# Kernel optimization log

Hardware: AMD Instinct MI355X
Metric: run time of the kernel (lower is better)

Reference implementation:

```python
import jax, jax.numpy as jnp
import numpy as np

B, T, D, HD = 4, 4096, 1024, 64

def setup_inputs() -> dict:
    key = jax.random.key(0)
    k1, k2, k3, k4 = jax.random.split(key, 4)
    scale = 1.0 / np.sqrt(D)
    return {
        "x": jax.random.normal(k1, (B, T, D), dtype=jnp.float32),
        "Wq": jax.random.normal(k2, (HD, D), dtype=jnp.float32) * scale,
        "Wk": jax.random.normal(k3, (HD, D), dtype=jnp.float32) * scale,
        "Wv": jax.random.normal(k4, (HD, D), dtype=jnp.float32) * scale,
    }

def reference(x, Wq, Wk, Wv):
    # x: [B,T,D]; W*: [head_dim, D] (torch Linear weight layout)
    Q = jnp.einsum('btd,hd->bth', x, Wq)  # [B,T,HD]
    K = jnp.einsum('btd,hd->bth', x, Wk)
    V = jnp.einsum('btd,hd->bth', x, Wv)
    hd = Q.shape[-1]
    scores = jnp.einsum('bqh,bkh->bqk', Q, K) * (hd ** -0.5)  # [B,T,T]
    t = scores.shape[1]
    causal = jnp.tril(jnp.ones((t, t), dtype=bool))
    scores = jnp.where(causal, scores, -jnp.inf)
    att = jax.nn.softmax(scores, axis=-1)
    return jnp.einsum('bqk,bkh->bqh', att, V)  # [B,T,HD]
```

## Files before the change

kernel.cpp:

```cpp
#include <hip/hip_runtime.h>
#include <stdint.h>

#define B_  4
#define T_  4096
#define D_  1024
#define HD_ 64
#define BT_ 16384

typedef short bf16x8 __attribute__((ext_vector_type(8)));
typedef float f32x4  __attribute__((ext_vector_type(4)));
typedef float f32x16 __attribute__((ext_vector_type(16)));
typedef unsigned short u16;
typedef u16 u16x4 __attribute__((ext_vector_type(4)));
typedef unsigned int u32;
typedef u32 u32x4 __attribute__((ext_vector_type(4)));

#define M0L2_  11.54156032f
#define QSCALE_ 0.18033688f

#define CPB_   264
#define NSLOT_ (4 * CPB_ * 2)

__device__ __forceinline__ u16 f2bf(float f) {
    union { float f; unsigned u; } v; v.f = f;
    unsigned r = (v.u + 0x7FFF + ((v.u >> 16) & 1)) >> 16;
    return (u16)r;
}
__device__ __forceinline__ float bf2f(u16 u) {
    union { unsigned u; float f; } v; v.u = ((unsigned)u) << 16;
    return v.f;
}
__device__ __forceinline__ u32 cvt_pk_bf16(float lo, float hi) {
    u32 r;
    asm("v_cvt_pk_bf16_f32 %0, %1, %2" : "=v"(r) : "v"(lo), "v"(hi));
    return r;
}

__global__ __launch_bounds__(256) void wconv_kernel(
    const float* __restrict__ wq, const float* __restrict__ wk,
    const float* __restrict__ wv, u16* __restrict__ wb)
{
    const int j   = blockIdx.x >> 5;
    const int off = (blockIdx.x & 31) * 2048 + threadIdx.x * 8;
    const float* src = (j == 0) ? wq : ((j == 1) ? wk : wv);
    f32x4 a0 = *(const f32x4*)(src + off);
    f32x4 a1 = *(const f32x4*)(src + off + 4);
    u32x4 b;
    b[0] = cvt_pk_bf16(a0[0], a0[1]);
    b[1] = cvt_pk_bf16(a0[2], a0[3]);
    b[2] = cvt_pk_bf16(a1[0], a1[1]);
    b[3] = cvt_pk_bf16(a1[2], a1[3]);
    *(u32x4*)(wb + j * 65536 + off) = b;
}

__global__ __launch_bounds__(256) void qkv_kernel(
    const float* __restrict__ x, const u16* __restrict__ wb,
    u16* __restrict__ qs, u16* __restrict__ kss, u16* __restrict__ vssT)
{
    __shared__ __align__(16) u16 xt[32][72];
    __shared__ __align__(16) u16 wt[192][72];

    const int tid  = threadIdx.x;
    const int lane = tid & 63;
    const int w    = tid >> 6;
    const int quad = lane >> 4;
    const int l16  = lane & 15;
    const int row0 = blockIdx.x * 32;
    const int sp   = w >> 1;
    const int gh   = (w & 1) * 6;

    const int xrow = tid >> 3;
    const int xcg  = tid & 7;

    f32x4 acc[6];
    #pragma unroll
    for (int g = 0; g < 6; ++g) acc[g] = (f32x4)0.0f;

    f32x4 xa, xb;
    bf16x8 wr[6];
    {
        const float* xp = x + (size_t)(row0 + xrow) * D_ + xcg * 8;
        xa = *(const f32x4*)xp; xb = *(const f32x4*)(xp + 4);
        #pragma unroll
        for (int i = 0; i < 6; ++i) {
            int chunk = tid + 256 * i;
            wr[i] = *(const bf16x8*)(wb + (size_t)(chunk >> 3) * D_ + (chunk & 7) * 8);
        }
    }

    for (int kc = 0; kc < 16; ++kc) {
        __syncthreads();
        {
            u32x4 px;
            px[0] = cvt_pk_bf16(xa[0], xa[1]);
            px[1] = cvt_pk_bf16(xa[2], xa[3]);
            px[2] = cvt_pk_bf16(xb[0], xb[1]);
            px[3] = cvt_pk_bf16(xb[2], xb[3]);
            *(u32x4*)&xt[xrow][xcg * 8] = px;
            #pragma unroll
            for (int i = 0; i < 6; ++i) {
                int chunk = tid + 256 * i;
                *(bf16x8*)&wt[chunk >> 3][(chunk & 7) * 8] = wr[i];
            }
        }
        __syncthreads();
        if (kc < 15) {
            const float* xp = x + (size_t)(row0 + xrow) * D_ + (kc + 1) * 64 + xcg * 8;
            xa = *(const f32x4*)xp; xb = *(const f32x4*)(xp + 4);
            #pragma unroll
            for (int i = 0; i < 6; ++i) {
                int chunk = tid + 256 * i;
                wr[i] = *(const bf16x8*)(wb + (size_t)(chunk >> 3) * D_ + (kc + 1) * 64 + (chunk & 7) * 8);
            }
        }
        #pragma unroll
        for (int ks = 0; ks < 2; ++ks) {
            bf16x8 a = *(const bf16x8*)&xt[sp * 16 + l16][ks * 32 + quad * 8];
            #pragma unroll
            for (int g = 0; g < 6; ++g) {
                bf16x8 b = *(const bf16x8*)&wt[(gh + g) * 16 + l16][ks * 32 + quad * 8];
                acc[g] = __builtin_amdgcn_mfma_f32_16x16x32_bf16(a, b, acc[g], 0, 0, 0);
            }
        }
    }
    #pragma unroll
    for (int g = 0; g < 6; ++g) {
        const int n = (gh + g) * 16 + l16;
        const int j = n >> 6, h = n & 63;
        const int rbase = row0 + sp * 16 + quad * 4;
        if (j == 0) {
            #pragma unroll
            for (int r = 0; r < 4; ++r) qs[(size_t)(rbase + r) * HD_ + h] = f2bf(acc[g][r] * QSCALE_);
        } else if (j == 1) {
            #pragma unroll
            for (int r = 0; r < 4; ++r) kss[(size_t)(rbase + r) * HD_ + h] = f2bf(acc[g][r]);
        } else {
            u16x4 v;
            #pragma unroll
            for (int r = 0; r < 4; ++r) v[r] = f2bf(acc[g][r]);
            *(u16x4*)(vssT + (size_t)h * BT_ + rbase) = v;
        }
    }
}

__global__ __launch_bounds__(256, 4) void attn_kernel(
    const u16* __restrict__ qs, const u16* __restrict__ kss,
    const u16* __restrict__ vssT,
    float* __restrict__ pl, u16* __restrict__ pO)
{
    __shared__ __align__(16) u16 kt2[8 * 65 * 8];
    __shared__ __align__(16) u16 vt2[8 * 65 * 8];

    const int m = blockIdx.x % CPB_;
    const int b = blockIdx.x / CPB_;

    int t0, bound, qtA, qtB;
    if (m < 240)      { int u = m >> 4; t0 = (m & 15) * 4; bound = 2 * u + 2; qtA = u;  qtB = 30 - u; }
    else if (m < 248) { t0 = (m - 240) * 4; bound = 1 << 30; qtA = 15; qtB = 15; }
    else              { t0 = (m - 248) * 4; bound = 1 << 30; qtA = 31; qtB = 31; }

    const int tid  = threadIdx.x;
    const int lane = tid & 63;
    const int w    = tid >> 6;
    const int l31  = lane & 31;
    const int hi   = lane >> 5;
    const size_t base = (size_t)b * T_;

    int qt    = (t0 < bound) ? qtA : qtB;
    int kti   = (t0 < bound) ? t0 : (t0 - bound);
    int qrow0 = qt * 128 + w * 32;

    bf16x8 qf[4];
    #pragma unroll
    for (int ds = 0; ds < 4; ++ds)
        qf[ds] = *(const bf16x8*)(qs + (base + qrow0 + l31) * HD_ + ds * 16 + hi * 8);

    f32x16 o0 = (f32x16)0.0f, o1 = (f32x16)0.0f;
    float l_acc = 0.0f;

    const int srow = tid >> 2, q4 = tid & 3;
    const u16* kp = kss  + (base + srow) * HD_ + q4 * 16;
    const u16* vp = vssT + (size_t)srow * BT_ + base + q4 * 16;
    u16* kdst = kt2 + ((((srow >> 5) * 4 + q4) * 65 + (srow & 31)) * 8);
    u16* vdst = vt2 + ((((srow >> 5) * 4 + q4) * 65 + (srow & 31)) * 8);

    bf16x8 kr0, kr1, vr0, vr1;
    {
        const u16* k0 = kp + (size_t)kti * 64 * HD_;
        kr0 = *(const bf16x8*)k0; kr1 = *(const bf16x8*)(k0 + 8);
        const u16* v0 = vp + kti * 64;
        vr0 = *(const bf16x8*)v0; vr1 = *(const bf16x8*)(v0 + 8);
    }

    auto FLUSH = [&](int role) {
        const int slot = (b * CPB_ + m) * 2 + role;
        u32 la = __builtin_bit_cast(u32, l_acc), lb = la;
        asm("v_permlane32_swap_b32 %0, %1" : "+v"(la), "+v"(lb));
        float lfull = __builtin_bit_cast(float, la) + __builtin_bit_cast(float, lb);
        if (hi == 0) pl[slot * 128 + w * 32 + l31] = lfull;
        #pragma unroll
        for (int reg = 0; reg < 16; ++reg) {
            int row = w * 32 + (reg & 3) + 8 * (reg >> 2) + 4 * hi;
            pO[(size_t)slot * 8192 + row * 64 + l31]      = f2bf(o0[reg]);
            pO[(size_t)slot * 8192 + row * 64 + 32 + l31] = f2bf(o1[reg]);
        }
    };

    for (int step = 0; step < 4; ++step) {
        const int i = t0 + step;
        __syncthreads();
        *(bf16x8*)(kdst)       = kr0;
        *(bf16x8*)(kdst + 256) = kr1;
        *(bf16x8*)(vdst)       = vr0;
        *(bf16x8*)(vdst + 256) = vr1;
        __syncthreads();

        int kti_next = 0;
        if (step < 3) {
            kti_next = (i + 1 < bound) ? (i + 1) : (i + 1 - bound);
            const u16* k0 = kp + (size_t)kti_next * 64 * HD_;
            kr0 = *(const bf16x8*)k0; kr1 = *(const bf16x8*)(k0 + 8);
            const u16* v0 = vp + kti_next * 64;
            vr0 = *(const bf16x8*)v0; vr1 = *(const bf16x8*)(v0 + 8);
        }

        if (kti * 64 <= qrow0 + 31) {
            const bool diag = (kti * 64 + 63 > qrow0);
            const int  qa   = qrow0 + l31;
            u32 wv[16];
            #pragma unroll
            for (int kg = 0; kg < 2; ++kg) {
                f32x16 s = (f32x16)0.0f;
                __builtin_amdgcn_s_setprio(1);
                #pragma unroll
                for (int ds = 0; ds < 4; ++ds) {
                    bf16x8 af = *(const bf16x8*)(kt2 + ((kg * 4 + ds) * 65 + lane) * 8);
                    s = __builtin_amdgcn_mfma_f32_32x32x16_bf16(af, qf[ds], s, 0, 0, 0);
                }
                __builtin_amdgcn_s_setprio(0);
                float lp = 0.0f;
                #pragma unroll
                for (int rp = 0; rp < 8; ++rp) {
                    float e0 = __builtin_amdgcn_exp2f(s[2 * rp]     - M0L2_);
                    float e1 = __builtin_amdgcn_exp2f(s[2 * rp + 1] - M0L2_);
                    if (diag) {
                        const int k0e = kti * 64 + kg * 32 + ((2 * rp) & 3) + 8 * ((2 * rp) >> 2) + 4 * hi;
                        if (k0e > qa)     e0 = 0.0f;
                        if (k0e + 1 > qa) e1 = 0.0f;
                    }
                    lp += e0 + e1;
                    wv[kg * 8 + rp] = cvt_pk_bf16(e0, e1);
                }
                l_acc += lp;
            }
            bf16x8 pa[4];
            #pragma unroll
            for (int ks = 0; ks < 4; ++ks) {
                const int kg2 = ks >> 1, k1 = ks & 1;
                u32 x0 = wv[kg2 * 8 + k1 * 4 + 0], y0 = wv[kg2 * 8 + k1 * 4 + 2];
                u32 x1 = wv[kg2 * 8 + k1 * 4 + 1], y1 = wv[kg2 * 8 + k1 * 4 + 3];
                asm("v_permlane32_swap_b32 %0, %1" : "+v"(x0), "+v"(y0));
                asm("v_permlane32_swap_b32 %0, %1" : "+v"(x1), "+v"(y1));
                u32x4 t; t[0] = x0; t[1] = x1; t[2] = y0; t[3] = y1;
                pa[ks] = __builtin_bit_cast(bf16x8, t);
            }
            __builtin_amdgcn_s_setprio(1);
            #pragma unroll
            for (int ks = 0; ks < 4; ++ks) {
                bf16x8 vf0 = *(const bf16x8*)(vt2 + ((0 * 4 + ks) * 65 + lane) * 8);
                o0 = __builtin_amdgcn_mfma_f32_32x32x16_bf16(pa[ks], vf0, o0, 0, 0, 0);
                bf16x8 vf1 = *(const bf16x8*)(vt2 + ((1 * 4 + ks) * 65 + lane) * 8);
                o1 = __builtin_amdgcn_mfma_f32_32x32x16_bf16(pa[ks], vf1, o1, 0, 0, 0);
            }
            __builtin_amdgcn_s_setprio(0);
        }

        kti = kti_next;
        if (step < 3 && (i + 1) == bound) {
            FLUSH(0);
            o0 = (f32x16)0.0f; o1 = (f32x16)0.0f; l_acc = 0.0f;
            qt = qtB; qrow0 = qt * 128 + w * 32;
            #pragma unroll
            for (int ds = 0; ds < 4; ++ds)
                qf[ds] = *(const bf16x8*)(qs + (base + qrow0 + l31) * HD_ + ds * 16 + hi * 8);
        }
    }
    FLUSH((t0 + 3 >= bound) ? 1 : 0);
}

__global__ __launch_bounds__(256) void merge_kernel(
    const float* __restrict__ pl, const u16* __restrict__ pO,
    float* __restrict__ out)
{
    const int bi  = blockIdx.x;
    const int rh  = bi & 1;
    const int qt2 = (bi >> 1) & 31;
    const int b   = bi >> 6;

    int c0, c1, role, mbase;
    if (qt2 <= 14)      { int u = qt2;      c0 = 0;                 c1 = (2 * u + 1) >> 2; role = 0; mbase = u * 16; }
    else if (qt2 == 15) { c0 = 0;           c1 = 7;                 role = 0; mbase = 240; }
    else if (qt2 <= 30) { int u = 30 - qt2; c0 = (2 * u + 2) >> 2;  c1 = 15; role = 1; mbase = u * 16; }
    else                { c0 = 0;           c1 = 15;                role = 0; mbase = 248; }

    const int row = rh * 64 + (threadIdx.x >> 2);
    const int hg  = (threadIdx.x & 3) * 16;

    float L = 0.0f;
    float o[16];
    #pragma unroll
    for (int i = 0; i < 16; ++i) o[i] = 0.0f;
    for (int c = c0; c <= c1; ++c) {
        const int slot = (b * CPB_ + mbase + c) * 2 + role;
        L += pl[slot * 128 + row];
        const u16* p = pO + (size_t)slot * 8192 + row * 64 + hg;
        bf16x8 v0 = *(const bf16x8*)p;
        bf16x8 v1 = *(const bf16x8*)(p + 8);
        #pragma unroll
        for (int i = 0; i < 8; ++i) { o[i] += bf2f((u16)v0[i]); o[8 + i] += bf2f((u16)v1[i]); }
    }
    const float inv = 1.0f / L;
    float* op = out + ((size_t)b * T_ + qt2 * 128 + row) * HD_ + hg;
    #pragma unroll
    for (int j = 0; j < 4; ++j) {
        f32x4 v;
        #pragma unroll
        for (int i = 0; i < 4; ++i) v[i] = o[j * 4 + i] * inv;
        *(f32x4*)(op + j * 4) = v;
    }
}

extern "C" void kernel_launch(void* const* d_in, const int* in_sizes, int n_in,
                              void* d_out, int out_size, void* d_ws, size_t ws_size,
                              hipStream_t stream) {
    const float* x  = (const float*)d_in[0];
    const float* wq = (const float*)d_in[1];
    const float* wk = (const float*)d_in[2];
    const float* wv = (const float*)d_in[3];

    const size_t NE = (size_t)BT_ * HD_;
    char* ws = (char*)d_ws;
    u16* qs   = (u16*)ws;
    u16* kss  = qs  + NE;
    u16* vssT = kss + NE;
    u16* wb   = vssT + NE;
    float* pl = (float*)(wb + 192 * 1024);
    u16* pO   = (u16*)(pl + (size_t)NSLOT_ * 128);
    float* out = (float*)d_out;

    wconv_kernel<<<dim3(96),        dim3(256), 0, stream>>>(wq, wk, wv, wb);
    qkv_kernel  <<<dim3(512),       dim3(256), 0, stream>>>(x, wb, qs, kss, vssT);
    attn_kernel <<<dim3(4 * CPB_),  dim3(256), 0, stream>>>(qs, kss, vssT, pl, pO);
    merge_kernel<<<dim3(256),       dim3(256), 0, stream>>>(pl, pO, out);
}
```

Baseline: 146.8 us.

## Pre-swizzle QKV weights into MFMA fragment order and drop LDS staging

The weight conversion kernel now writes bf16 weights directly in the per-lane MFMA B-fragment layout. The QKV projection kernel then loads its A fragments from global x and its B fragments from the swizzled weights straight into registers, with no shared-memory tiles or __syncthreads. The next k-chunk is prefetched into registers. This removes LDS traffic and barriers, but every wave now reloads the weights itself, and x is read with a less coalesced 16-row by 32-byte pattern.

```diff
diff --git a/kernel.cpp b/kernel.cpp
--- a/kernel.cpp
+++ b/kernel.cpp
@@ -40,26 +40,29 @@
     const float* __restrict__ wq, const float* __restrict__ wk,
     const float* __restrict__ wv, u16* __restrict__ wb)
 {
-    const int j   = blockIdx.x >> 5;
-    const int off = (blockIdx.x & 31) * 2048 + threadIdx.x * 8;
-    const float* src = (j == 0) ? wq : ((j == 1) ? wk : wv);
-    f32x4 a0 = *(const f32x4*)(src + off);
-    f32x4 a1 = *(const f32x4*)(src + off + 4);
+    const int cid  = blockIdx.x * 256 + threadIdx.x;
+    const int n    = cid >> 7;
+    const int koct = cid & 127;
+    const int mat  = n >> 6;
+    const int row  = n & 63;
+    const float* src = (mat == 0) ? wq : ((mat == 1) ? wk : wv);
+    const float* p = src + row * 1024 + koct * 8;
+    f32x4 a0 = *(const f32x4*)p;
+    f32x4 a1 = *(const f32x4*)(p + 4);
     u32x4 b;
     b[0] = cvt_pk_bf16(a0[0], a0[1]);
     b[1] = cvt_pk_bf16(a0[2], a0[3]);
     b[2] = cvt_pk_bf16(a1[0], a1[1]);
     b[3] = cvt_pk_bf16(a1[2], a1[3]);
-    *(u32x4*)(wb + j * 65536 + off) = b;
+    const int kc  = koct >> 3, ksl = (koct >> 2) & 1, qd = koct & 3;
+    const int f   = (kc * 12 + (n >> 4)) * 2 + ksl;
+    *(u32x4*)(wb + (size_t)(f * 64 + qd * 16 + (n & 15)) * 8) = b;
 }
 
 __global__ __launch_bounds__(256) void qkv_kernel(
     const float* __restrict__ x, const u16* __restrict__ wb,
     u16* __restrict__ qs, u16* __restrict__ kss, u16* __restrict__ vssT)
 {
-    __shared__ __align__(16) u16 xt[32][72];
-    __shared__ __align__(16) u16 wt[192][72];
-
     const int tid  = threadIdx.x;
     const int lane = tid & 63;
     const int w    = tid >> 6;
@@ -69,58 +72,60 @@
     const int sp   = w >> 1;
     const int gh   = (w & 1) * 6;
 
-    const int xrow = tid >> 3;
-    const int xcg  = tid & 7;
-
     f32x4 acc[6];
     #pragma unroll
     for (int g = 0; g < 6; ++g) acc[g] = (f32x4)0.0f;
 
-    f32x4 xa, xb;
-    bf16x8 wr[6];
-    {
-        const float* xp = x + (size_t)(row0 + xrow) * D_ + xcg * 8;
-        xa = *(const f32x4*)xp; xb = *(const f32x4*)(xp + 4);
-        #pragma unroll
-        for (int i = 0; i < 6; ++i) {
-            int chunk = tid + 256 * i;
-            wr[i] = *(const bf16x8*)(wb + (size_t)(chunk >> 3) * D_ + (chunk & 7) * 8);
-        }
-    }
+    const float* xq = x + (size_t)(row0 + sp * 16 + l16) * D_ + quad * 8;
+    const u16*   wp = wb + (size_t)lane * 8;
+
+    f32x4 xr[4]; bf16x8 wc[12];
+    #pragma unroll
+    for (int ks = 0; ks < 2; ++ks) {
+        xr[ks * 2]     = *(const f32x4*)(xq + ks * 32);
+        xr[ks * 2 + 1] = *(const f32x4*)(xq + ks * 32 + 4);
+    }
+    #pragma unroll
+    for (int g = 0; g < 6; ++g)
+        #pragma unroll
+        for (int ks = 0; ks < 2; ++ks)
+            wc[g * 2 + ks] = *(const bf16x8*)(wp + (size_t)((gh + g) * 2 + ks) * 512);
 
     for (int kc = 0; kc < 16; ++kc) {
-        __syncthreads();
-        {
+        f32x4 xn[4]; bf16x8 wn[12];
+        if (kc < 15) {
+            const float* xq1 = xq + (kc + 1) * 64;
+            #pragma unroll
+            for (int ks = 0; ks < 2; ++ks) {
+                xn[ks * 2]     = *(const f32x4*)(xq1 + ks * 32);
+                xn[ks * 2 + 1] = *(const f32x4*)(xq1 + ks * 32 + 4);
+            }
+            #pragma unroll
+            for (int g = 0; g < 6; ++g)
+                #pragma unroll
+                for (int ks = 0; ks < 2; ++ks)
+                    wn[g * 2 + ks] = *(const bf16x8*)(wp + (size_t)((kc + 1) * 24 + (gh + g) * 2 + ks) * 512);
+        }
+        bf16x8 a[2];
+        #pragma unroll
+        for (int ks = 0; ks < 2; ++ks) {
             u32x4 px;
-            px[0] = cvt_pk_bf16(xa[0], xa[1]);
-            px[1] = cvt_pk_bf16(xa[2], xa[3]);
-            px[2] = cvt_pk_bf16(xb[0], xb[1]);
-            px[3] = cvt_pk_bf16(xb[2], xb[3]);
-            *(u32x4*)&xt[xrow][xcg * 8] = px;
-            #pragma unroll
-            for (int i = 0; i < 6; ++i) {
-                int chunk = tid + 256 * i;
-                *(bf16x8*)&wt[chunk >> 3][(chunk & 7) * 8] = wr[i];
-            }
-        }
-        __syncthreads();
+            px[0] = cvt_pk_bf16(xr[ks * 2][0], xr[ks * 2][1]);
+            px[1] = cvt_pk_bf16(xr[ks * 2][2], xr[ks * 2][3]);
+            px[2] = cvt_pk_bf16(xr[ks * 2 + 1][0], xr[ks * 2 + 1][1]);
+            px[3] = cvt_pk_bf16(xr[ks * 2 + 1][2], xr[ks * 2 + 1][3]);
+            a[ks] = __builtin_bit_cast(bf16x8, px);
+        }
+        #pragma unroll
+        for (int ks = 0; ks < 2; ++ks)
+            #pragma unroll
+            for (int g = 0; g < 6; ++g)
+                acc[g] = __builtin_amdgcn_mfma_f32_16x16x32_bf16(a[ks], wc[g * 2 + ks], acc[g], 0, 0, 0);
         if (kc < 15) {
-            const float* xp = x + (size_t)(row0 + xrow) * D_ + (kc + 1) * 64 + xcg * 8;
-            xa = *(const f32x4*)xp; xb = *(const f32x4*)(xp + 4);
-            #pragma unroll
-            for (int i = 0; i < 6; ++i) {
-                int chunk = tid + 256 * i;
-                wr[i] = *(const bf16x8*)(wb + (size_t)(chunk >> 3) * D_ + (kc + 1) * 64 + (chunk & 7) * 8);
-            }
-        }
-        #pragma unroll
-        for (int ks = 0; ks < 2; ++ks) {
-            bf16x8 a = *(const bf16x8*)&xt[sp * 16 + l16][ks * 32 + quad * 8];
-            #pragma unroll
-            for (int g = 0; g < 6; ++g) {
-                bf16x8 b = *(const bf16x8*)&wt[(gh + g) * 16 + l16][ks * 32 + quad * 8];
-                acc[g] = __builtin_amdgcn_mfma_f32_16x16x32_bf16(a, b, acc[g], 0, 0, 0);
-            }
+            #pragma unroll
+            for (int i = 0; i < 4; ++i)  xr[i] = xn[i];
+            #pragma unroll
+            for (int i = 0; i < 12; ++i) wc[i] = wn[i];
         }
     }
     #pragma unroll
```

Measured after the change: 155.9 us. 1.06x slower.

## Enlarge QKV projection tile to 64 rows with 512-thread blocks

Applied to the files above, without the earlier changes.

The QKV projection kernel now handles 64 rows per block with 8 waves instead of 32 rows with 4 waves, and the grid shrinks from 512 to 256 blocks. Each wave computes a 2x3 tile of MFMA outputs, reusing each weight fragment across two row subtiles. Because the weight tile is shared by twice as many rows, global weight traffic per output row is halved. The cost is fewer blocks on the device, which may underfill the CUs, and more LDS per block.

```diff
diff --git a/kernel.cpp b/kernel.cpp
--- a/kernel.cpp
+++ b/kernel.cpp
@@ -53,11 +53,11 @@
     *(u32x4*)(wb + j * 65536 + off) = b;
 }
 
-__global__ __launch_bounds__(256) void qkv_kernel(
+__global__ __launch_bounds__(512) void qkv_kernel(
     const float* __restrict__ x, const u16* __restrict__ wb,
     u16* __restrict__ qs, u16* __restrict__ kss, u16* __restrict__ vssT)
 {
-    __shared__ __align__(16) u16 xt[32][72];
+    __shared__ __align__(16) u16 xt[64][72];
     __shared__ __align__(16) u16 wt[192][72];
 
     const int tid  = threadIdx.x;
@@ -65,25 +65,27 @@
     const int w    = tid >> 6;
     const int quad = lane >> 4;
     const int l16  = lane & 15;
-    const int row0 = blockIdx.x * 32;
-    const int sp   = w >> 1;
-    const int gh   = (w & 1) * 6;
+    const int row0 = blockIdx.x * 64;
+    const int rh   = w >> 2;
+    const int ct   = w & 3;
 
     const int xrow = tid >> 3;
     const int xcg  = tid & 7;
 
-    f32x4 acc[6];
-    #pragma unroll
-    for (int g = 0; g < 6; ++g) acc[g] = (f32x4)0.0f;
+    f32x4 acc[2][3];
+    #pragma unroll
+    for (int s = 0; s < 2; ++s)
+        #pragma unroll
+        for (int g = 0; g < 3; ++g) acc[s][g] = (f32x4)0.0f;
 
     f32x4 xa, xb;
-    bf16x8 wr[6];
+    bf16x8 wr[3];
     {
         const float* xp = x + (size_t)(row0 + xrow) * D_ + xcg * 8;
         xa = *(const f32x4*)xp; xb = *(const f32x4*)(xp + 4);
         #pragma unroll
-        for (int i = 0; i < 6; ++i) {
-            int chunk = tid + 256 * i;
+        for (int i = 0; i < 3; ++i) {
+            int chunk = tid + 512 * i;
             wr[i] = *(const bf16x8*)(wb + (size_t)(chunk >> 3) * D_ + (chunk & 7) * 8);
         }
     }
@@ -98,8 +100,8 @@
             px[3] = cvt_pk_bf16(xb[2], xb[3]);
             *(u32x4*)&xt[xrow][xcg * 8] = px;
             #pragma unroll
-            for (int i = 0; i < 6; ++i) {
-                int chunk = tid + 256 * i;
+            for (int i = 0; i < 3; ++i) {
+                int chunk = tid + 512 * i;
                 *(bf16x8*)&wt[chunk >> 3][(chunk & 7) * 8] = wr[i];
             }
         }
@@ -108,37 +110,45 @@
             const float* xp = x + (size_t)(row0 + xrow) * D_ + (kc + 1) * 64 + xcg * 8;
             xa = *(const f32x4*)xp; xb = *(const f32x4*)(xp + 4);
             #pragma unroll
-            for (int i = 0; i < 6; ++i) {
-                int chunk = tid + 256 * i;
+            for (int i = 0; i < 3; ++i) {
+                int chunk = tid + 512 * i;
                 wr[i] = *(const bf16x8*)(wb + (size_t)(chunk >> 3) * D_ + (kc + 1) * 64 + (chunk & 7) * 8);
             }
         }
         #pragma unroll
         for (int ks = 0; ks < 2; ++ks) {
-            bf16x8 a = *(const bf16x8*)&xt[sp * 16 + l16][ks * 32 + quad * 8];
-            #pragma unroll
-            for (int g = 0; g < 6; ++g) {
-                bf16x8 b = *(const bf16x8*)&wt[(gh + g) * 16 + l16][ks * 32 + quad * 8];
-                acc[g] = __builtin_amdgcn_mfma_f32_16x16x32_bf16(a, b, acc[g], 0, 0, 0);
-            }
-        }
-    }
-    #pragma unroll
-    for (int g = 0; g < 6; ++g) {
-        const int n = (gh + g) * 16 + l16;
-        const int j = n >> 6, h = n & 63;
-        const int rbase = row0 + sp * 16 + quad * 4;
-        if (j == 0) {
-            #pragma unroll
-            for (int r = 0; r < 4; ++r) qs[(size_t)(rbase + r) * HD_ + h] = f2bf(acc[g][r] * QSCALE_);
-        } else if (j == 1) {
-            #pragma unroll
-            for (int r = 0; r < 4; ++r) kss[(size_t)(rbase + r) * HD_ + h] = f2bf(acc[g][r]);
-        } else {
-            u16x4 v;
-            #pragma unroll
-            for (int r = 0; r < 4; ++r) v[r] = f2bf(acc[g][r]);
-            *(u16x4*)(vssT + (size_t)h * BT_ + rbase) = v;
+            bf16x8 a[2];
+            #pragma unroll
+            for (int s = 0; s < 2; ++s)
+                a[s] = *(const bf16x8*)&xt[rh * 32 + s * 16 + l16][ks * 32 + quad * 8];
+            #pragma unroll
+            for (int g = 0; g < 3; ++g) {
+                bf16x8 bfr = *(const bf16x8*)&wt[(ct * 3 + g) * 16 + l16][ks * 32 + quad * 8];
+                #pragma unroll
+                for (int s = 0; s < 2; ++s)
+                    acc[s][g] = __builtin_amdgcn_mfma_f32_16x16x32_bf16(a[s], bfr, acc[s][g], 0, 0, 0);
+            }
+        }
+    }
+    #pragma unroll
+    for (int s = 0; s < 2; ++s) {
+        #pragma unroll
+        for (int g = 0; g < 3; ++g) {
+            const int n = (ct * 3 + g) * 16 + l16;
+            const int j = n >> 6, h = n & 63;
+            const int rbase = row0 + rh * 32 + s * 16 + quad * 4;
+            if (j == 0) {
+                #pragma unroll
+                for (int r = 0; r < 4; ++r) qs[(size_t)(rbase + r) * HD_ + h] = f2bf(acc[s][g][r] * QSCALE_);
+            } else if (j == 1) {
+                #pragma unroll
+                for (int r = 0; r < 4; ++r) kss[(size_t)(rbase + r) * HD_ + h] = f2bf(acc[s][g][r]);
+            } else {
+                u16x4 v;
+                #pragma unroll
+                for (int r = 0; r < 4; ++r) v[r] = f2bf(acc[s][g][r]);
+                *(u16x4*)(vssT + (size_t)h * BT_ + rbase) = v;
+            }
         }
     }
 }
@@ -349,7 +359,7 @@
     float* out = (float*)d_out;
 
     wconv_kernel<<<dim3(96),        dim3(256), 0, stream>>>(wq, wk, wv, wb);
-    qkv_kernel  <<<dim3(512),       dim3(256), 0, stream>>>(x, wb, qs, kss, vssT);
+    qkv_kernel  <<<dim3(256),       dim3(512), 0, stream>>>(x, wb, qs, kss, vssT);
     attn_kernel <<<dim3(4 * CPB_),  dim3(256), 0, stream>>>(qs, kss, vssT, pl, pO);
     merge_kernel<<<dim3(256),       dim3(256), 0, stream>>>(pl, pO, out);
 }
```

Result: slower. 150.9 us (+2.8%).
